# Kernel tuning notes

Measured on AMD Instinct MI355X. Metric: run time of the kernel, lower is better.

The kernel has to match this reference:

```python
import jax, jax.numpy as jnp
import numpy as np

B, N_Z, NOISE_DIM, STATE_DIM, HIDDEN_DIM, CLASS_NUM = 2048, 8, 32, 1024, 1024, 1
EPI_HIDDEN = 512
PRIOR_H = 5
IN_FEATURES = NOISE_DIM + STATE_DIM + HIDDEN_DIM  # 2080
OUT_FEATURES = NOISE_DIM * CLASS_NUM  # 32
POSTERIOR_SCALE = 1.0
PRIOR_SCALE = 1.0


def _xavier(key, shape):
    fan_in, fan_out = shape[-2], shape[-1]
    std = np.sqrt(2.0 / (fan_in + fan_out)).astype(np.float32)
    return jax.random.normal(key, shape, dtype=jnp.float32) * std


def setup_inputs() -> dict:
    key = jax.random.key(0)
    ks = jax.random.split(key, 10)
    x = jax.random.normal(ks[0], (B, STATE_DIM), dtype=jnp.float32)
    feature = jax.random.normal(ks[1], (B, HIDDEN_DIM), dtype=jnp.float32)
    z = jax.random.normal(ks[2], (B, N_Z, NOISE_DIM), dtype=jnp.float32)
    # epinet: Linear(IN_FEATURES->EPI_HIDDEN), ReLU, Linear(EPI_HIDDEN->OUT_FEATURES)
    Wep1 = _xavier(ks[3], (IN_FEATURES, EPI_HIDDEN))
    bep1 = jnp.zeros((EPI_HIDDEN,), dtype=jnp.float32)
    Wep2 = _xavier(ks[4], (EPI_HIDDEN, OUT_FEATURES))
    bep2 = jnp.zeros((OUT_FEATURES,), dtype=jnp.float32)
    # priornet: ensemble of NOISE_DIM MLPs state_dim->5->5->class_num (frozen)
    Wp1 = _xavier(ks[5], (NOISE_DIM, STATE_DIM, PRIOR_H))
    bp1 = jnp.zeros((NOISE_DIM, PRIOR_H), dtype=jnp.float32)
    Wp2 = _xavier(ks[6], (NOISE_DIM, PRIOR_H, PRIOR_H))
    bp2 = jnp.zeros((NOISE_DIM, PRIOR_H), dtype=jnp.float32)
    Wp3 = _xavier(ks[7], (NOISE_DIM, PRIOR_H, CLASS_NUM))
    bp3 = jnp.zeros((NOISE_DIM, CLASS_NUM), dtype=jnp.float32)
    return {"x": x, "feature": feature, "z": z,
            "Wep1": Wep1, "bep1": bep1, "Wep2": Wep2, "bep2": bep2,
            "Wp1": Wp1, "bp1": bp1, "Wp2": Wp2, "bp2": bp2, "Wp3": Wp3, "bp3": bp3}


def reference(x, feature, z, Wep1, bep1, Wep2, bep2, Wp1, bp1, Wp2, bp2, Wp3, bp3):
    batch = x.shape[0]
    n = z.shape[1]
    # [B, state+hidden] -> broadcast over n z-samples, concat z -> [B, n, IN_FEATURES]
    xf = jnp.concatenate([x, feature], axis=-1)
    epinet_inp = jnp.concatenate(
        [jnp.broadcast_to(xf[:, None, :], (batch, n, xf.shape[-1])), z], axis=-1)
    # small epinet MLP
    h = jax.nn.relu(jnp.einsum('bnd,dh->bnh', epinet_inp, Wep1) + bep1)
    out = jnp.einsum('bnh,ho->bno', h, Wep2) + bep2  # [B, n, noise_dim*class_num]
    out = out.reshape(batch, n, NOISE_DIM, CLASS_NUM)
    out = jnp.einsum('bsna,bsn->bsa', out, z)  # [B, n, class_num]
    # ensemble prior: NOISE_DIM tiny MLPs, vectorized as batched GEMMs
    h1 = jax.nn.relu(jnp.einsum('bi,eih->beh', x, Wp1) + bp1)
    h2 = jax.nn.relu(jnp.einsum('beh,ehg->beg', h1, Wp2) + bp2)
    p = jnp.einsum('beg,egc->bec', h2, Wp3) + bp3  # [B, ensemble=noise_dim, class_num]
    prior_out = jnp.einsum('bzc,bnz->bnc', p, z)  # [B, n, class_num]
    return out * POSTERIOR_SCALE + prior_out * PRIOR_SCALE
```

## Files before the change

### kernel.cpp

```cpp
#include <hip/hip_runtime.h>
#include <hip/hip_bf16.h>


typedef __hip_bfloat16 bf16;
typedef __attribute__((ext_vector_type(8))) short short8;
typedef __attribute__((ext_vector_type(4))) float f32x4;

#define NCOMB 768
#define NSPLIT 4
#define A_BYTES  (2048u * 2048u * 2u)
#define WT_BYTES (768u * 2048u * 2u)

__device__ __forceinline__ void gload_lds16(const bf16* g, bf16* l) {
    __builtin_amdgcn_global_load_lds(
        (const __attribute__((address_space(1))) void*)g,
        (__attribute__((address_space(3))) void*)l, 16, 0, 0);
}

__device__ __forceinline__ short f2bf_bits(float f) {
    bf16 h = __float2bfloat16(f);
    return *reinterpret_cast<short*>(&h);
}

__global__ __launch_bounds__(256) void prep_a(const float* __restrict__ x,
                                              const float* __restrict__ feat,
                                              bf16* __restrict__ A) {
    int idx = blockIdx.x * 256 + threadIdx.x;
    int b = idx >> 9;
    int g = idx & 511;
    const float* src = (g < 256) ? (x + (size_t)b * 1024 + g * 4)
                                 : (feat + (size_t)b * 1024 + (g - 256) * 4);
    float4 v = *(const float4*)src;
    short4 p;
    p.x = f2bf_bits(v.x); p.y = f2bf_bits(v.y);
    p.z = f2bf_bits(v.z); p.w = f2bf_bits(v.w);
    *(short4*)(A + (size_t)b * 2048 + g * 4) = p;
}

__global__ __launch_bounds__(256) void prep_wt(const float* __restrict__ Wep1,
                                               const float* __restrict__ Wp1,
                                               bf16* __restrict__ WT) {
    const int t = threadIdx.x;
    if (blockIdx.x < 256) {
        __shared__ short tile[64 * 66];
        int kt = blockIdx.x >> 3, nt = blockIdx.x & 7;
        int k0 = kt * 64, n0 = nt * 64;
        int r = t >> 4, cq = t & 15;
#pragma unroll
        for (int i = 0; i < 4; ++i) {
            int rr = r + i * 16;
            float4 v = *(const float4*)(Wep1 + (size_t)(k0 + rr) * 512 + n0 + cq * 4);
            tile[(cq * 4 + 0) * 66 + rr] = f2bf_bits(v.x);
            tile[(cq * 4 + 1) * 66 + rr] = f2bf_bits(v.y);
            tile[(cq * 4 + 2) * 66 + rr] = f2bf_bits(v.z);
            tile[(cq * 4 + 3) * 66 + rr] = f2bf_bits(v.w);
        }
        __syncthreads();
#pragma unroll
        for (int i = 0; i < 2; ++i) {
            int ch = i * 256 + t;
            int nr = ch >> 3, kc = ch & 7;
            short8 s = *(const short8*)(tile + nr * 66 + kc * 8);
            *(short8*)(WT + (size_t)(n0 + nr) * 2048 + k0 + kc * 8) = s;
        }
    } else {
        int local = (blockIdx.x - 256) * 256 + t;
        int n = 512 + (local >> 11);
        int k = local & 2047;
        float v = 0.f;
        if (n < 672) {
            int q = n - 512;
            int e = q / 5, h = q - e * 5;
            if (k < 1024) v = Wp1[(size_t)e * 5120 + k * 5 + h];
        }
        WT[(size_t)n * 2048 + k] = __float2bfloat16(v);
    }
}

__global__ __launch_bounds__(256) void gemm_split(const bf16* __restrict__ A,
                                                  const bf16* __restrict__ WT,
                                                  float* __restrict__ Gp) {
    __shared__ bf16 As[128 * 64];
    __shared__ bf16 Bs[128 * 64];
    const int t    = threadIdx.x;
    const int lane = t & 63;
    const int wv   = t >> 6;
    const int m0 = blockIdx.y * 128;
    const int n0 = blockIdx.x * 128;
    const int kbase = blockIdx.z * 512;
    const int lm = lane & 15;
    const int lq = lane >> 4;
    const int wm = (wv & 1) * 64;
    const int wn = (wv >> 1) * 64;
    f32x4 acc[4][4] = {};

    for (int k0 = 0; k0 < 512; k0 += 64) {
        __syncthreads();
#pragma unroll
        for (int i = 0; i < 4; ++i) {
            int chunk = i * 256 + wv * 64 + lane;
            int row   = chunk >> 3;
            int gph   = chunk & 7;
            int gda   = gph ^ (row & 7);
            gload_lds16(A  + (size_t)(m0 + row) * 2048 + kbase + k0 + gda * 8,
                        As + (i * 256 + wv * 64) * 8);
            gload_lds16(WT + (size_t)(n0 + row) * 2048 + kbase + k0 + gda * 8,
                        Bs + (i * 256 + wv * 64) * 8);
        }
        __syncthreads();
#pragma unroll
        for (int kk = 0; kk < 64; kk += 32) {
            short8 af[4], bfr[4];
#pragma unroll
            for (int i2 = 0; i2 < 4; ++i2) {
                int ra = wm + i2 * 16 + lm;
                int ga = ((kk >> 3) + lq) ^ (ra & 7);
                af[i2] = *(const short8*)(As + ra * 64 + ga * 8);
                int rb = wn + i2 * 16 + lm;
                int gb = ((kk >> 3) + lq) ^ (rb & 7);
                bfr[i2] = *(const short8*)(Bs + rb * 64 + gb * 8);
            }
#pragma unroll
            for (int mi = 0; mi < 4; ++mi)
#pragma unroll
                for (int ni = 0; ni < 4; ++ni)
                    acc[mi][ni] = __builtin_amdgcn_mfma_f32_16x16x32_bf16(
                        af[mi], bfr[ni], acc[mi][ni], 0, 0, 0);
        }
    }
    float* Gs = Gp + (size_t)blockIdx.z * 2048 * NCOMB;
#pragma unroll
    for (int mi = 0; mi < 4; ++mi)
#pragma unroll
        for (int ni = 0; ni < 4; ++ni) {
            int row = m0 + wm + mi * 16 + lq * 4;
            int col = n0 + wn + ni * 16 + lm;
#pragma unroll
            for (int r = 0; r < 4; ++r)
                Gs[(size_t)(row + r) * NCOMB + col] = acc[mi][ni][r];
        }
}

__global__ __launch_bounds__(256) void combine(const float* __restrict__ Gp,
                                               const float* __restrict__ z,
                                               const float* __restrict__ Wep1,
                                               const float* __restrict__ Wep2,
                                               const float* __restrict__ bep1,
                                               const float* __restrict__ bep2,
                                               const float* __restrict__ bp1,
                                               const float* __restrict__ Wp2,
                                               const float* __restrict__ bp2,
                                               const float* __restrict__ Wp3,
                                               const float* __restrict__ bp3,
                                               float* __restrict__ out) {
    __shared__ float zf[1024];
    __shared__ short zbf[1024];
    __shared__ float hxs[4 * 512];
    __shared__ float h1s[640];
    __shared__ float h2s[640];
    __shared__ float ps[128];
    __shared__ short WzB[256 * 32];
    __shared__ short W2B[32 * 256];
    __shared__ short hB[32 * 256];
    __shared__ float o2s[1024];
    const int t = threadIdx.x, bg = blockIdx.x;
    const int lane = t & 63, wv = t >> 6;
    const int lm = lane & 15, lq = lane >> 4;
    const int mt = wv & 1;
    const int jt = wv >> 1;
    const size_t SSTR = (size_t)2048 * NCOMB;

    {
        float4 v = *(const float4*)(z + (size_t)bg * 1024 + t * 4);
        zf[t * 4 + 0] = v.x; zf[t * 4 + 1] = v.y; zf[t * 4 + 2] = v.z; zf[t * 4 + 3] = v.w;
        zbf[t * 4 + 0] = f2bf_bits(v.x); zbf[t * 4 + 1] = f2bf_bits(v.y);
        zbf[t * 4 + 2] = f2bf_bits(v.z); zbf[t * 4 + 3] = f2bf_bits(v.w);
    }
#pragma unroll
    for (int g = 0; g < 2; ++g) {
        int q = g * 256 + t;
        int bi = q >> 7, cq = q & 127;
        const float* gp = Gp + (size_t)(bg * 4 + bi) * NCOMB + cq * 4;
        float4 s0 = *(const float4*)(gp);
        float4 s1 = *(const float4*)(gp + SSTR);
        float4 s2 = *(const float4*)(gp + 2 * SSTR);
        float4 s3 = *(const float4*)(gp + 3 * SSTR);
        float4 bb = *(const float4*)(bep1 + cq * 4);
        hxs[bi * 512 + cq * 4 + 0] = s0.x + s1.x + s2.x + s3.x + bb.x;
        hxs[bi * 512 + cq * 4 + 1] = s0.y + s1.y + s2.y + s3.y + bb.y;
        hxs[bi * 512 + cq * 4 + 2] = s0.z + s1.z + s2.z + s3.z + bb.z;
        hxs[bi * 512 + cq * 4 + 3] = s0.w + s1.w + s2.w + s3.w + bb.w;
    }
    if (t < 160) {
        float bv = bp1[t];
#pragma unroll
        for (int bi = 0; bi < 4; ++bi) {
            const float* gp = Gp + (size_t)(bg * 4 + bi) * NCOMB + 512 + t;
            float v = gp[0] + gp[SSTR] + gp[2 * SSTR] + gp[3 * SSTR] + bv;
            h1s[bi * 160 + t] = fmaxf(v, 0.f);
        }
    }
    __syncthreads();
    if (t < 160) {
        int e = t / 5, g5 = t - e * 5;
#pragma unroll
        for (int bi = 0; bi < 4; ++bi) {
            float a = bp2[t];
#pragma unroll
            for (int h = 0; h < 5; ++h)
                a += h1s[bi * 160 + e * 5 + h] * Wp2[e * 25 + h * 5 + g5];
            h2s[bi * 160 + t] = fmaxf(a, 0.f);
        }
    }
    __syncthreads();
    if (t < 128) {
        int bi = t >> 5, j = t & 31;
        float a = bp3[j];
#pragma unroll
        for (int g = 0; g < 5; ++g)
            a += h2s[bi * 160 + j * 5 + g] * Wp3[j * 5 + g];
        ps[bi * 32 + j] = a;
    }

    f32x4 o2acc = {};
    for (int half = 0; half < 2; ++half) {
        __syncthreads();
#pragma unroll
        for (int i = 0; i < 8; ++i) {
            int idx = i * 256 + t;
            int k = idx >> 6, cq = idx & 63;
            int ch = cq * 4;
            float4 v = *(const float4*)(Wep1 + (size_t)(2048 + k) * 512 + half * 256 + ch);
            int kg = k >> 3, kl = k & 7;
            WzB[(ch + 0) * 32 + (kg ^ (((ch + 0) >> 1) & 3)) * 8 + kl] = f2bf_bits(v.x);
            WzB[(ch + 1) * 32 + (kg ^ (((ch + 1) >> 1) & 3)) * 8 + kl] = f2bf_bits(v.y);
            WzB[(ch + 2) * 32 + (kg ^ (((ch + 2) >> 1) & 3)) * 8 + kl] = f2bf_bits(v.z);
            WzB[(ch + 3) * 32 + (kg ^ (((ch + 3) >> 1) & 3)) * 8 + kl] = f2bf_bits(v.w);
        }
#pragma unroll
        for (int i = 0; i < 8; ++i) {
            int idx = i * 256 + t;
            int c = idx >> 3, jq = idx & 7;
            float4 v = *(const float4*)(Wep2 + (size_t)(half * 256 + c) * 32 + jq * 4);
            int cg = c >> 3, cl = c & 7;
            W2B[(jq * 4 + 0) * 256 + (cg ^ (jq * 4 + 0)) * 8 + cl] = f2bf_bits(v.x);
            W2B[(jq * 4 + 1) * 256 + (cg ^ (jq * 4 + 1)) * 8 + cl] = f2bf_bits(v.y);
            W2B[(jq * 4 + 2) * 256 + (cg ^ (jq * 4 + 2)) * 8 + cl] = f2bf_bits(v.z);
            W2B[(jq * 4 + 3) * 256 + (cg ^ (jq * 4 + 3)) * 8 + cl] = f2bf_bits(v.w);
        }
        __syncthreads();
        short8 afz = *(const short8*)(zbf + (mt * 16 + lm) * 32 + lq * 8);
#pragma unroll
        for (int u = 0; u < 8; ++u) {
            int nt = jt * 8 + u;
            int crow = nt * 16 + lm;
            short8 bfz = *(const short8*)(WzB + crow * 32 + (lq ^ ((crow >> 1) & 3)) * 8);
            f32x4 az = {};
            az = __builtin_amdgcn_mfma_f32_16x16x32_bf16(afz, bfz, az, 0, 0, 0);
            int cfull = half * 256 + crow;
            int cg = crow >> 3, cl = crow & 7;
#pragma unroll
            for (int r = 0; r < 4; ++r) {
                int row = mt * 16 + lq * 4 + r;
                float hv = fmaxf(hxs[(row >> 3) * 512 + cfull] + az[r], 0.f);
                hB[row * 256 + (cg ^ row) * 8 + cl] = f2bf_bits(hv);
            }
        }
        __syncthreads();
        {
            int arow = mt * 16 + lm;
            int jrow = jt * 16 + lm;
#pragma unroll
            for (int ks = 0; ks < 8; ++ks) {
                int dg = ks * 4 + lq;
                short8 a2 = *(const short8*)(hB + arow * 256 + (dg ^ arow) * 8);
                short8 b2 = *(const short8*)(W2B + jrow * 256 + (dg ^ jrow) * 8);
                o2acc = __builtin_amdgcn_mfma_f32_16x16x32_bf16(a2, b2, o2acc, 0, 0, 0);
            }
        }
    }
#pragma unroll
    for (int r = 0; r < 4; ++r)
        o2s[(mt * 16 + lq * 4 + r) * 32 + jt * 16 + lm] = o2acc[r];
    __syncthreads();
    {
        int r = t >> 3, jg = t & 7;
        float val = 0.f;
#pragma unroll
        for (int u = 0; u < 4; ++u) {
            int j = jg * 4 + u;
            val += (o2s[r * 32 + j] + ps[(r >> 3) * 32 + j]) * zf[r * 32 + j];
        }
        val += __shfl_xor(val, 1, 64);
        val += __shfl_xor(val, 2, 64);
        val += __shfl_xor(val, 4, 64);
        if ((t & 7) == 0) out[(size_t)bg * 32 + r] = val;
    }
}

extern "C" void kernel_launch(void* const* d_in, const int* in_sizes, int n_in,
                              void* d_out, int out_size, void* d_ws, size_t ws_size,
                              hipStream_t stream) {
    const float* x    = (const float*)d_in[0];
    const float* feat = (const float*)d_in[1];
    const float* z    = (const float*)d_in[2];
    const float* Wep1 = (const float*)d_in[3];
    const float* bep1 = (const float*)d_in[4];
    const float* Wep2 = (const float*)d_in[5];
    const float* bep2 = (const float*)d_in[6];
    const float* Wp1  = (const float*)d_in[7];
    const float* bp1  = (const float*)d_in[8];
    const float* Wp2  = (const float*)d_in[9];
    const float* bp2  = (const float*)d_in[10];
    const float* Wp3  = (const float*)d_in[11];
    const float* bp3  = (const float*)d_in[12];
    float* out = (float*)d_out;
    (void)bep2;

    char* ws  = (char*)d_ws;
    bf16* A   = (bf16*)ws;
    bf16* WT  = (bf16*)(ws + A_BYTES);
    float* Gp = (float*)(ws + A_BYTES + WT_BYTES);

    prep_a<<<4096, 256, 0, stream>>>(x, feat, A);
    prep_wt<<<2304, 256, 0, stream>>>(Wep1, Wp1, WT);
    gemm_split<<<dim3(6, 16, NSPLIT), 256, 0, stream>>>(A, WT, Gp);
    combine<<<512, 256, 0, stream>>>(Gp, z, Wep1, Wep2, bep1, bep2,
                                     bp1, Wp2, bp2, Wp3, bp3, out);
}
```

Measured before the change: 126.1 us.

## Precompute small epinet weights in bf16, merge prep kernels, deepen split-K

The two prep kernels become one launch. That launch also converts the z-part of Wep1 and all of Wep2 to transposed bf16 once, so every combine block no longer re-reads and converts them. The split-K GEMM goes from 4 to 8 splits, the grid axes are swapped, and stores of all-zero padding and prior columns are skipped. Combine now sums 8 partials and runs the hidden layer in one pass instead of two halves. The cost is more partial-sum traffic through the workspace.

Measured after the change: 117.3 us. 7.0% less time.

```diff
diff --git a/kernel.cpp b/kernel.cpp
--- a/kernel.cpp
+++ b/kernel.cpp
@@ -7,9 +7,11 @@
 typedef __attribute__((ext_vector_type(4))) float f32x4;
 
 #define NCOMB 768
-#define NSPLIT 4
-#define A_BYTES  (2048u * 2048u * 2u)
-#define WT_BYTES (768u * 2048u * 2u)
+#define NSPLIT 8
+#define A_BYTES   (2048u * 2048u * 2u)
+#define WT_BYTES  (768u * 2048u * 2u)
+#define WZT_BYTES (512u * 32u * 2u)
+#define W2T_BYTES (32u * 512u * 2u)
 
 __device__ __forceinline__ void gload_lds16(const bf16* g, bf16* l) {
     __builtin_amdgcn_global_load_lds(
@@ -22,58 +24,80 @@
     return *reinterpret_cast<short*>(&h);
 }
 
-__global__ __launch_bounds__(256) void prep_a(const float* __restrict__ x,
-                                              const float* __restrict__ feat,
-                                              bf16* __restrict__ A) {
-    int idx = blockIdx.x * 256 + threadIdx.x;
-    int b = idx >> 9;
-    int g = idx & 511;
-    const float* src = (g < 256) ? (x + (size_t)b * 1024 + g * 4)
-                                 : (feat + (size_t)b * 1024 + (g - 256) * 4);
-    float4 v = *(const float4*)src;
-    short4 p;
-    p.x = f2bf_bits(v.x); p.y = f2bf_bits(v.y);
-    p.z = f2bf_bits(v.z); p.w = f2bf_bits(v.w);
-    *(short4*)(A + (size_t)b * 2048 + g * 4) = p;
-}
-
-__global__ __launch_bounds__(256) void prep_wt(const float* __restrict__ Wep1,
-                                               const float* __restrict__ Wp1,
-                                               bf16* __restrict__ WT) {
+__global__ __launch_bounds__(256) void prep(const float* __restrict__ x,
+                                            const float* __restrict__ feat,
+                                            const float* __restrict__ Wep1,
+                                            const float* __restrict__ Wep2,
+                                            const float* __restrict__ Wp1,
+                                            bf16* __restrict__ A,
+                                            bf16* __restrict__ WT,
+                                            bf16* __restrict__ WzT,
+                                            bf16* __restrict__ W2T) {
     const int t = threadIdx.x;
-    if (blockIdx.x < 256) {
-        __shared__ short tile[64 * 66];
-        int kt = blockIdx.x >> 3, nt = blockIdx.x & 7;
-        int k0 = kt * 64, n0 = nt * 64;
-        int r = t >> 4, cq = t & 15;
-#pragma unroll
-        for (int i = 0; i < 4; ++i) {
-            int rr = r + i * 16;
-            float4 v = *(const float4*)(Wep1 + (size_t)(k0 + rr) * 512 + n0 + cq * 4);
-            tile[(cq * 4 + 0) * 66 + rr] = f2bf_bits(v.x);
-            tile[(cq * 4 + 1) * 66 + rr] = f2bf_bits(v.y);
-            tile[(cq * 4 + 2) * 66 + rr] = f2bf_bits(v.z);
-            tile[(cq * 4 + 3) * 66 + rr] = f2bf_bits(v.w);
-        }
-        __syncthreads();
+    const int blk = blockIdx.x;
+    if (blk < 4096) {
+        int idx = blk * 256 + t;
+        int b = idx >> 9;
+        int g = idx & 511;
+        const float* src = (g < 256) ? (x + (size_t)b * 1024 + g * 4)
+                                     : (feat + (size_t)b * 1024 + (g - 256) * 4);
+        float4 v = *(const float4*)src;
+        short4 p;
+        p.x = f2bf_bits(v.x); p.y = f2bf_bits(v.y);
+        p.z = f2bf_bits(v.z); p.w = f2bf_bits(v.w);
+        *(short4*)(A + (size_t)b * 2048 + g * 4) = p;
+    } else if (blk < 6400) {
+        int wb = blk - 4096;
+        if (wb < 256) {
+            __shared__ short tile[64 * 66];
+            int kt = wb >> 3, nt = wb & 7;
+            int k0 = kt * 64, n0 = nt * 64;
+            int r = t >> 4, cq = t & 15;
+#pragma unroll
+            for (int i = 0; i < 4; ++i) {
+                int rr = r + i * 16;
+                float4 v = *(const float4*)(Wep1 + (size_t)(k0 + rr) * 512 + n0 + cq * 4);
+                tile[(cq * 4 + 0) * 66 + rr] = f2bf_bits(v.x);
+                tile[(cq * 4 + 1) * 66 + rr] = f2bf_bits(v.y);
+                tile[(cq * 4 + 2) * 66 + rr] = f2bf_bits(v.z);
+                tile[(cq * 4 + 3) * 66 + rr] = f2bf_bits(v.w);
+            }
+            __syncthreads();
+#pragma unroll
+            for (int i = 0; i < 2; ++i) {
+                int ch = i * 256 + t;
+                int nr = ch >> 3, kc = ch & 7;
+                short8 s = *(const short8*)(tile + nr * 66 + kc * 8);
+                *(short8*)(WT + (size_t)(n0 + nr) * 2048 + k0 + kc * 8) = s;
+            }
+        } else {
+            int local = (wb - 256) * 256 + t;
+            int n = 512 + (local >> 11);
+            int k = local & 2047;
+            float v = 0.f;
+            if (n < 672) {
+                int q = n - 512;
+                int e = q / 5, h = q - e * 5;
+                if (k < 1024) v = Wp1[(size_t)e * 5120 + k * 5 + h];
+            }
+            WT[(size_t)n * 2048 + k] = __float2bfloat16(v);
+        }
+    } else if (blk < 6432) {
+        int local = (blk - 6400) * 256 + t;
 #pragma unroll
         for (int i = 0; i < 2; ++i) {
-            int ch = i * 256 + t;
-            int nr = ch >> 3, kc = ch & 7;
-            short8 s = *(const short8*)(tile + nr * 66 + kc * 8);
-            *(short8*)(WT + (size_t)(n0 + nr) * 2048 + k0 + kc * 8) = s;
+            int e = i * 8192 + local;
+            int c = e >> 5, k = e & 31;
+            WzT[e] = __float2bfloat16(Wep1[(size_t)(2048 + k) * 512 + c]);
         }
     } else {
-        int local = (blockIdx.x - 256) * 256 + t;
-        int n = 512 + (local >> 11);
-        int k = local & 2047;
-        float v = 0.f;
-        if (n < 672) {
-            int q = n - 512;
-            int e = q / 5, h = q - e * 5;
-            if (k < 1024) v = Wp1[(size_t)e * 5120 + k * 5 + h];
-        }
-        WT[(size_t)n * 2048 + k] = __float2bfloat16(v);
+        int local = (blk - 6432) * 256 + t;
+#pragma unroll
+        for (int i = 0; i < 2; ++i) {
+            int e = i * 8192 + local;
+            int j = e >> 9, c = e & 511;
+            W2T[e] = __float2bfloat16(Wep2[(size_t)c * 32 + j]);
+        }
     }
 }
 
@@ -85,16 +109,16 @@
     const int t    = threadIdx.x;
     const int lane = t & 63;
     const int wv   = t >> 6;
-    const int m0 = blockIdx.y * 128;
-    const int n0 = blockIdx.x * 128;
-    const int kbase = blockIdx.z * 512;
+    const int m0 = blockIdx.x * 128;
+    const int n0 = blockIdx.y * 128;
+    const int kbase = blockIdx.z * 256;
     const int lm = lane & 15;
     const int lq = lane >> 4;
     const int wm = (wv & 1) * 64;
     const int wn = (wv >> 1) * 64;
     f32x4 acc[4][4] = {};
 
-    for (int k0 = 0; k0 < 512; k0 += 64) {
+    for (int k0 = 0; k0 < 256; k0 += 64) {
         __syncthreads();
 #pragma unroll
         for (int i = 0; i < 4; ++i) {
@@ -128,6 +152,7 @@
                         af[mi], bfr[ni], acc[mi][ni], 0, 0, 0);
         }
     }
+    const bool zhi = blockIdx.z >= 4;
     float* Gs = Gp + (size_t)blockIdx.z * 2048 * NCOMB;
 #pragma unroll
     for (int mi = 0; mi < 4; ++mi)
@@ -135,16 +160,18 @@
         for (int ni = 0; ni < 4; ++ni) {
             int row = m0 + wm + mi * 16 + lq * 4;
             int col = n0 + wn + ni * 16 + lm;
-#pragma unroll
-            for (int r = 0; r < 4; ++r)
-                Gs[(size_t)(row + r) * NCOMB + col] = acc[mi][ni][r];
+            if (col < 672 && !(zhi && col >= 512)) {
+#pragma unroll
+                for (int r = 0; r < 4; ++r)
+                    Gs[(size_t)(row + r) * NCOMB + col] = acc[mi][ni][r];
+            }
         }
 }
 
 __global__ __launch_bounds__(256) void combine(const float* __restrict__ Gp,
                                                const float* __restrict__ z,
-                                               const float* __restrict__ Wep1,
-                                               const float* __restrict__ Wep2,
+                                               const bf16* __restrict__ WzT,
+                                               const bf16* __restrict__ W2T,
                                                const float* __restrict__ bep1,
                                                const float* __restrict__ bep2,
                                                const float* __restrict__ bp1,
@@ -155,13 +182,11 @@
                                                float* __restrict__ out) {
     __shared__ float zf[1024];
     __shared__ short zbf[1024];
-    __shared__ float hxs[4 * 512];
+    __shared__ float hxs[2048];
     __shared__ float h1s[640];
     __shared__ float h2s[640];
     __shared__ float ps[128];
-    __shared__ short WzB[256 * 32];
-    __shared__ short W2B[32 * 256];
-    __shared__ short hB[32 * 256];
+    __shared__ short hB[32 * 512];
     __shared__ float o2s[1024];
     const int t = threadIdx.x, bg = blockIdx.x;
     const int lane = t & 63, wv = t >> 6;
@@ -181,15 +206,13 @@
         int q = g * 256 + t;
         int bi = q >> 7, cq = q & 127;
         const float* gp = Gp + (size_t)(bg * 4 + bi) * NCOMB + cq * 4;
-        float4 s0 = *(const float4*)(gp);
-        float4 s1 = *(const float4*)(gp + SSTR);
-        float4 s2 = *(const float4*)(gp + 2 * SSTR);
-        float4 s3 = *(const float4*)(gp + 3 * SSTR);
-        float4 bb = *(const float4*)(bep1 + cq * 4);
-        hxs[bi * 512 + cq * 4 + 0] = s0.x + s1.x + s2.x + s3.x + bb.x;
-        hxs[bi * 512 + cq * 4 + 1] = s0.y + s1.y + s2.y + s3.y + bb.y;
-        hxs[bi * 512 + cq * 4 + 2] = s0.z + s1.z + s2.z + s3.z + bb.z;
-        hxs[bi * 512 + cq * 4 + 3] = s0.w + s1.w + s2.w + s3.w + bb.w;
+        float4 a4 = *(const float4*)(bep1 + cq * 4);
+#pragma unroll
+        for (int s = 0; s < 8; ++s) {
+            float4 v = *(const float4*)(gp + (size_t)s * SSTR);
+            a4.x += v.x; a4.y += v.y; a4.z += v.z; a4.w += v.w;
+        }
+        *(float4*)(hxs + bi * 512 + cq * 4) = a4;
     }
     if (t < 160) {
         float bv = bp1[t];
@@ -221,62 +244,32 @@
             a += h2s[bi * 160 + j * 5 + g] * Wp3[j * 5 + g];
         ps[bi * 32 + j] = a;
     }
-
+    short8 afz = *(const short8*)(zbf + (mt * 16 + lm) * 32 + lq * 8);
+#pragma unroll
+    for (int u = 0; u < 16; ++u) {
+        int crow = (jt * 16 + u) * 16 + lm;
+        short8 bfz = *(const short8*)(WzT + crow * 32 + lq * 8);
+        f32x4 az = {};
+        az = __builtin_amdgcn_mfma_f32_16x16x32_bf16(afz, bfz, az, 0, 0, 0);
+        int cg = crow >> 3, cl = crow & 7;
+#pragma unroll
+        for (int r = 0; r < 4; ++r) {
+            int row = mt * 16 + lq * 4 + r;
+            float hv = fmaxf(hxs[(row >> 3) * 512 + crow] + az[r], 0.f);
+            hB[row * 512 + ((cg ^ row)) * 8 + cl] = f2bf_bits(hv);
+        }
+    }
+    __syncthreads();
     f32x4 o2acc = {};
-    for (int half = 0; half < 2; ++half) {
-        __syncthreads();
-#pragma unroll
-        for (int i = 0; i < 8; ++i) {
-            int idx = i * 256 + t;
-            int k = idx >> 6, cq = idx & 63;
-            int ch = cq * 4;
-            float4 v = *(const float4*)(Wep1 + (size_t)(2048 + k) * 512 + half * 256 + ch);
-            int kg = k >> 3, kl = k & 7;
-            WzB[(ch + 0) * 32 + (kg ^ (((ch + 0) >> 1) & 3)) * 8 + kl] = f2bf_bits(v.x);
-            WzB[(ch + 1) * 32 + (kg ^ (((ch + 1) >> 1) & 3)) * 8 + kl] = f2bf_bits(v.y);
-            WzB[(ch + 2) * 32 + (kg ^ (((ch + 2) >> 1) & 3)) * 8 + kl] = f2bf_bits(v.z);
-            WzB[(ch + 3) * 32 + (kg ^ (((ch + 3) >> 1) & 3)) * 8 + kl] = f2bf_bits(v.w);
-        }
-#pragma unroll
-        for (int i = 0; i < 8; ++i) {
-            int idx = i * 256 + t;
-            int c = idx >> 3, jq = idx & 7;
-            float4 v = *(const float4*)(Wep2 + (size_t)(half * 256 + c) * 32 + jq * 4);
-            int cg = c >> 3, cl = c & 7;
-            W2B[(jq * 4 + 0) * 256 + (cg ^ (jq * 4 + 0)) * 8 + cl] = f2bf_bits(v.x);
-            W2B[(jq * 4 + 1) * 256 + (cg ^ (jq * 4 + 1)) * 8 + cl] = f2bf_bits(v.y);
-            W2B[(jq * 4 + 2) * 256 + (cg ^ (jq * 4 + 2)) * 8 + cl] = f2bf_bits(v.z);
-            W2B[(jq * 4 + 3) * 256 + (cg ^ (jq * 4 + 3)) * 8 + cl] = f2bf_bits(v.w);
-        }
-        __syncthreads();
-        short8 afz = *(const short8*)(zbf + (mt * 16 + lm) * 32 + lq * 8);
-#pragma unroll
-        for (int u = 0; u < 8; ++u) {
-            int nt = jt * 8 + u;
-            int crow = nt * 16 + lm;
-            short8 bfz = *(const short8*)(WzB + crow * 32 + (lq ^ ((crow >> 1) & 3)) * 8);
-            f32x4 az = {};
-            az = __builtin_amdgcn_mfma_f32_16x16x32_bf16(afz, bfz, az, 0, 0, 0);
-            int cfull = half * 256 + crow;
-            int cg = crow >> 3, cl = crow & 7;
-#pragma unroll
-            for (int r = 0; r < 4; ++r) {
-                int row = mt * 16 + lq * 4 + r;
-                float hv = fmaxf(hxs[(row >> 3) * 512 + cfull] + az[r], 0.f);
-                hB[row * 256 + (cg ^ row) * 8 + cl] = f2bf_bits(hv);
-            }
-        }
-        __syncthreads();
-        {
-            int arow = mt * 16 + lm;
-            int jrow = jt * 16 + lm;
-#pragma unroll
-            for (int ks = 0; ks < 8; ++ks) {
-                int dg = ks * 4 + lq;
-                short8 a2 = *(const short8*)(hB + arow * 256 + (dg ^ arow) * 8);
-                short8 b2 = *(const short8*)(W2B + jrow * 256 + (dg ^ jrow) * 8);
-                o2acc = __builtin_amdgcn_mfma_f32_16x16x32_bf16(a2, b2, o2acc, 0, 0, 0);
-            }
+    {
+        int arow = mt * 16 + lm;
+        int jrow = jt * 16 + lm;
+#pragma unroll
+        for (int ks = 0; ks < 16; ++ks) {
+            int dg = ks * 4 + lq;
+            short8 a2 = *(const short8*)(hB + arow * 512 + (dg ^ arow) * 8);
+            short8 b2 = *(const short8*)(W2T + jrow * 512 + dg * 8);
+            o2acc = __builtin_amdgcn_mfma_f32_16x16x32_bf16(a2, b2, o2acc, 0, 0, 0);
         }
     }
 #pragma unroll
@@ -289,7 +282,7 @@
 #pragma unroll
         for (int u = 0; u < 4; ++u) {
             int j = jg * 4 + u;
-            val += (o2s[r * 32 + j] + ps[(r >> 3) * 32 + j]) * zf[r * 32 + j];
+            val += (o2s[r * 32 + j] + bep2[j] + ps[(r >> 3) * 32 + j]) * zf[r * 32 + j];
         }
         val += __shfl_xor(val, 1, 64);
         val += __shfl_xor(val, 2, 64);
@@ -315,16 +308,16 @@
     const float* Wp3  = (const float*)d_in[11];
     const float* bp3  = (const float*)d_in[12];
     float* out = (float*)d_out;
-    (void)bep2;
 
     char* ws  = (char*)d_ws;
     bf16* A   = (bf16*)ws;
     bf16* WT  = (bf16*)(ws + A_BYTES);
-    float* Gp = (float*)(ws + A_BYTES + WT_BYTES);
-
-    prep_a<<<4096, 256, 0, stream>>>(x, feat, A);
-    prep_wt<<<2304, 256, 0, stream>>>(Wep1, Wp1, WT);
-    gemm_split<<<dim3(6, 16, NSPLIT), 256, 0, stream>>>(A, WT, Gp);
-    combine<<<512, 256, 0, stream>>>(Gp, z, Wep1, Wep2, bep1, bep2,
+    bf16* WzT = (bf16*)(ws + A_BYTES + WT_BYTES);
+    bf16* W2T = (bf16*)(ws + A_BYTES + WT_BYTES + WZT_BYTES);
+    float* Gp = (float*)(ws + A_BYTES + WT_BYTES + WZT_BYTES + W2T_BYTES);
+
+    prep<<<6464, 256, 0, stream>>>(x, feat, Wep1, Wep2, Wp1, A, WT, WzT, W2T);
+    gemm_split<<<dim3(16, 6, NSPLIT), 256, 0, stream>>>(A, WT, Gp);
+    combine<<<512, 256, 0, stream>>>(Gp, z, WzT, W2T, bep1, bep2,
                                      bp1, Wp2, bp2, Wp3, bp3, out);
 }
```
